# Optimization experiments

Measured on AMD Instinct MI355X. Metric: run time of the kernel, lower is better.

## Reference

```python
import jax, jax.numpy as jnp
import numpy as np

N_NODES = 100000
N_EDGES = 1000000
IN_DIM, HID_DIM, OUT_DIM = 64, 64, 128


def gcn_conv(x, W, b, src, dst, deg_inv_sqrt, n_nodes):
    # PyG GCNConv: x' = D^{-1/2} (A + I) D^{-1/2} (x W) + b
    xw = x @ W  # [N, out]
    norm = deg_inv_sqrt[src] * deg_inv_sqrt[dst]  # [E'] (edges incl. self-loops)
    msgs = xw[src] * norm[:, None]  # gather + scale, [E', out]
    out = jax.ops.segment_sum(msgs, dst, num_segments=n_nodes)
    return out + b


def setup_inputs() -> dict:
    key = jax.random.key(0)
    ks = jax.random.split(key, 8)
    x = jax.random.normal(ks[0], (N_NODES, IN_DIM), dtype=jnp.float32)
    edge_index = jax.random.randint(ks[1], (2, N_EDGES), 0, N_NODES, dtype=jnp.int64 if jax.config.read('jax_enable_x64') else jnp.int32)
    # Glorot-ish init for weights, zeros for biases (matches GCNConv defaults)
    def glorot(k, fan_in, fan_out):
        s = jnp.sqrt(6.0 / (fan_in + fan_out))
        return jax.random.uniform(k, (fan_in, fan_out), jnp.float32, -s, s)
    return {
        "x": x,
        "W1": glorot(ks[2], IN_DIM, HID_DIM), "b1": jnp.zeros((HID_DIM,), jnp.float32),
        "W2": glorot(ks[3], HID_DIM, HID_DIM), "b2": jnp.zeros((HID_DIM,), jnp.float32),
        "W3": glorot(ks[4], HID_DIM, OUT_DIM), "b3": jnp.zeros((OUT_DIM,), jnp.float32),
        "edge_index": edge_index,
    }


def reference(x, W1, b1, W2, b2, W3, b3, edge_index):
    n = x.shape[0]
    loop = jnp.arange(n, dtype=edge_index.dtype)
    src = jnp.concatenate([edge_index[0], loop])  # add self-loops
    dst = jnp.concatenate([edge_index[1], loop])
    deg = jax.ops.segment_sum(jnp.ones_like(dst, dtype=x.dtype), dst, num_segments=n)
    deg_inv_sqrt = jnp.where(deg > 0, jax.lax.rsqrt(deg), 0.0)
    # Dropout(p=0.5) is identity in eval mode
    h = jax.nn.relu(gcn_conv(x, W1, b1, src, dst, deg_inv_sqrt, n))
    h = jax.nn.relu(gcn_conv(h, W2, b2, src, dst, deg_inv_sqrt, n))
    return gcn_conv(h, W3, b3, src, dst, deg_inv_sqrt, n)
```

## Files before the change

### kernel.cpp

```cpp
#include <hip/hip_runtime.h>
#include <hip/hip_fp16.h>


#define NBMAX 512
#define EPB   4096


__global__ __launch_bounds__(256) void bin_hist(const int* __restrict__ dst,
                                                int* __restrict__ hist, int E, int NB) {
  __shared__ int cnt[NBMAX];
  for (int i = threadIdx.x; i < NB; i += 256) cnt[i] = 0;
  __syncthreads();
  int base = blockIdx.x * EPB;
  for (int it = 0; it < EPB; it += 256) {
    int e = base + it + threadIdx.x;
    if (e < E) atomicAdd(&cnt[dst[e] >> 8], 1);
  }
  __syncthreads();
  for (int i = threadIdx.x; i < NB; i += 256) hist[(size_t)blockIdx.x * NB + i] = cnt[i];
}

__global__ __launch_bounds__(256) void bucket_prefix(int* __restrict__ hist,
                                                     int* __restrict__ bucket_tot,
                                                     int nblk, int NB) {
  __shared__ int tmp[256];
  int b = blockIdx.x;
  int t = threadIdx.x;
  int v = (t < nblk) ? hist[(size_t)t * NB + b] : 0;
  tmp[t] = v;
  __syncthreads();
  for (int off = 1; off < 256; off <<= 1) {
    int a = (t >= off) ? tmp[t - off] : 0;
    __syncthreads();
    tmp[t] += a;
    __syncthreads();
  }
  if (t < nblk) hist[(size_t)t * NB + b] = tmp[t] - v;
  if (t == 255) bucket_tot[b] = tmp[255];
}

__global__ __launch_bounds__(512) void bucket_scan(const int* __restrict__ bucket_tot,
                                                   int* __restrict__ bucket_off, int NB, int E) {
  __shared__ int tmp[NBMAX];
  int t = threadIdx.x;
  int v = (t < NB) ? bucket_tot[t] : 0;
  tmp[t] = v;
  __syncthreads();
  for (int off = 1; off < 512; off <<= 1) {
    int a = (t >= off) ? tmp[t - off] : 0;
    __syncthreads();
    tmp[t] += a;
    __syncthreads();
  }
  if (t < NB) bucket_off[t] = tmp[t] - v;
  if (t == 0) bucket_off[NB] = E;
}

__global__ __launch_bounds__(256) void bin_scatter(const int* __restrict__ src,
                                                   const int* __restrict__ dst,
                                                   const int* __restrict__ chunk_excl,
                                                   const int* __restrict__ bucket_off,
                                                   int* __restrict__ pairs, int E, int NB) {
  __shared__ int cur[NBMAX];
  for (int i = threadIdx.x; i < NB; i += 256)
    cur[i] = bucket_off[i] + chunk_excl[(size_t)blockIdx.x * NB + i];
  __syncthreads();
  int base = blockIdx.x * EPB;
  for (int it = 0; it < EPB; it += 256) {
    int e = base + it + threadIdx.x;
    if (e < E) {
      int d = dst[e];
      int pos = atomicAdd(&cur[d >> 8], 1);
      pairs[pos] = src[e] | ((d & 255) << 17);
    }
  }
}

__device__ __forceinline__ unsigned int packh(float a, float b) {
  unsigned int lo = (unsigned int)__half_as_ushort(__float2half_rn(a));
  unsigned int hi = (unsigned int)__half_as_ushort(__float2half_rn(b));
  return lo | (hi << 16);
}

__device__ __forceinline__ void unpack_add(float& x0, float& x1, unsigned int u) {
  x0 += __half2float(__ushort_as_half((unsigned short)(u & 0xffffu)));
  x1 += __half2float(__ushort_as_half((unsigned short)(u >> 16)));
}

__global__ __launch_bounds__(256) void bucket_fill(const int* __restrict__ pairs,
                                                   const int* __restrict__ bucket_off,
                                                   int* __restrict__ row_ptr,
                                                   int* __restrict__ csr_src,
                                                   float* __restrict__ dis,
                                                   const float* __restrict__ x,
                                                   unsigned short* __restrict__ xs,
                                                   int n, int NB) {
  __shared__ int cnt[256];
  __shared__ int tmp[256];
  __shared__ int cur[256];
  __shared__ float sdis[256];
  int b = blockIdx.x;
  int t = threadIdx.x;
  int node_base = b << 8;
  int ebeg = bucket_off[b];
  int eend = bucket_off[b + 1];
  cnt[t] = 0;
  __syncthreads();
  for (int e = ebeg + t; e < eend; e += 256) {
    atomicAdd(&cnt[(pairs[e] >> 17) & 255], 1);
  }
  __syncthreads();
  int v = cnt[t];
  tmp[t] = v;
  __syncthreads();
  for (int off = 1; off < 256; off <<= 1) {
    int a = (t >= off) ? tmp[t - off] : 0;
    __syncthreads();
    tmp[t] += a;
    __syncthreads();
  }
  int excl = tmp[t] - v;
  int node = node_base + t;
  float s = rsqrtf((float)v + 1.0f);
  sdis[t] = s;
  if (node < n) {
    row_ptr[node] = ebeg + excl;
    dis[node] = s;
  }
  cur[t] = ebeg + excl;
  if (b == NB - 1 && t == 0) row_ptr[n] = eend;
  __syncthreads();
  for (int e = ebeg + t; e < eend; e += 256) {
    int p = pairs[e];
    int pos = atomicAdd(&cur[(p >> 17) & 255], 1);
    csr_src[pos] = p & 0x1FFFF;
  }
  int rows = n - node_base;
  if (rows > 256) rows = 256;
  for (int i = t; i < rows * 8; i += 256) {
    int r = i >> 3;
    float sc = sdis[r];
    const float4* p = (const float4*)(x + ((size_t)(node_base + r) * 64) + (i & 7) * 8);
    float4 f0 = p[0];
    float4 f1 = p[1];
    uint4 u;
    u.x = packh(f0.x * sc, f0.y * sc);
    u.y = packh(f0.z * sc, f0.w * sc);
    u.z = packh(f1.x * sc, f1.y * sc);
    u.w = packh(f1.z * sc, f1.w * sc);
    *(uint4*)(xs + (size_t)(node_base + r) * 64 + (i & 7) * 8) = u;
  }
}


template <bool RELU, bool SCALE, bool OUTH, int NCB>
__global__ __launch_bounds__(256, 4) void gcn_layer(
    const int* __restrict__ row_ptr, const int* __restrict__ csr_src,
    const unsigned short* __restrict__ in, const float* __restrict__ dis,
    const float* __restrict__ W, const float* __restrict__ Bv,
    float* __restrict__ yF, unsigned short* __restrict__ yH, int n) {
  __shared__ float Xs[64 * 68];
  __shared__ float Ws[64 * 64 * NCB];
  int tid = threadIdx.x;
  int rb = blockIdx.x * 64;

  for (int i = tid; i < 64 * 16 * NCB; i += 256) {
    int k = i / (16 * NCB);
    int cq = (i % (16 * NCB)) << 2;
    *(float4*)&Ws[k * (64 * NCB) + cq] = *(const float4*)&W[(size_t)k * (64 * NCB) + cq];
  }

  int l15 = tid & 15;
  int gbase = tid & 48;
  int grp = tid >> 4;
  for (int it = 0; it < 4; ++it) {
    int r = it * 16 + grp;
    int cl = min(rb + r, n - 1);
    int beg = row_ptr[cl];
    int end = row_ptr[cl + 1];

    float a0 = 0.f, a1 = 0.f, a2 = 0.f, a3 = 0.f;
    {
      uint2 q = *(const uint2*)(in + (size_t)cl * 64 + l15 * 4);
      unpack_add(a0, a1, q.x); unpack_add(a2, a3, q.y);
    }
    int k = beg;
    for (; k + 16 <= end; k += 16) {
      int idx = csr_src[k + l15];
#pragma unroll
      for (int rr = 0; rr < 16; rr += 2) {
        int s0 = __shfl(idx, gbase + rr);
        int s1 = __shfl(idx, gbase + rr + 1);
        uint2 q0 = *(const uint2*)(in + (size_t)s0 * 64 + l15 * 4);
        uint2 q1 = *(const uint2*)(in + (size_t)s1 * 64 + l15 * 4);
        unpack_add(a0, a1, q0.x); unpack_add(a2, a3, q0.y);
        unpack_add(a0, a1, q1.x); unpack_add(a2, a3, q1.y);
      }
    }
    int cnt = end - k;
    if (cnt > 0) {
      int ii = k + l15;
      int last = end - 1;
      ii = (ii < end) ? ii : last;
      int idx = csr_src[ii];
#pragma unroll
      for (int rr = 0; rr < 16; rr += 2) {
        int s0 = __shfl(idx, gbase + rr);
        int s1 = __shfl(idx, gbase + rr + 1);
        uint2 q0 = *(const uint2*)(in + (size_t)s0 * 64 + l15 * 4);
        uint2 q1 = *(const uint2*)(in + (size_t)s1 * 64 + l15 * 4);
        q0.x = (rr < cnt) ? q0.x : 0u;
        q0.y = (rr < cnt) ? q0.y : 0u;
        q1.x = (rr + 1 < cnt) ? q1.x : 0u;
        q1.y = (rr + 1 < cnt) ? q1.y : 0u;
        unpack_add(a0, a1, q0.x); unpack_add(a2, a3, q0.y);
        unpack_add(a0, a1, q1.x); unpack_add(a2, a3, q1.y);
      }
    }
    float sc = dis[cl];
    *(float4*)&Xs[r * 68 + l15 * 4] =
        make_float4(a0 * sc, a1 * sc, a2 * sc, a3 * sc);
  }
  __syncthreads();

  int r0 = (tid >> 4) << 2;
  int c0 = (tid & 15) << 2;
  int gr0 = rb + r0;

#pragma unroll
  for (int cb = 0; cb < NCB; ++cb) {
    float4 a0 = make_float4(0.f, 0.f, 0.f, 0.f);
    float4 a1 = a0, a2 = a0, a3 = a0;

#pragma unroll 2
    for (int kc = 0; kc < 64; kc += 4) {
      float4 x0 = *(const float4*)&Xs[(r0 + 0) * 68 + kc];
      float4 x1 = *(const float4*)&Xs[(r0 + 1) * 68 + kc];
      float4 x2 = *(const float4*)&Xs[(r0 + 2) * 68 + kc];
      float4 x3 = *(const float4*)&Xs[(r0 + 3) * 68 + kc];
      const float* wp = &Ws[(size_t)kc * (64 * NCB) + cb * 64 + c0];
      float4 w0 = *(const float4*)(wp + 0 * (64 * NCB));
      float4 w1 = *(const float4*)(wp + 1 * (64 * NCB));
      float4 w2 = *(const float4*)(wp + 2 * (64 * NCB));
      float4 w3 = *(const float4*)(wp + 3 * (64 * NCB));
      a0.x = fmaf(x0.x, w0.x, a0.x); a0.y = fmaf(x0.x, w0.y, a0.y);
      a0.z = fmaf(x0.x, w0.z, a0.z); a0.w = fmaf(x0.x, w0.w, a0.w);
      a0.x = fmaf(x0.y, w1.x, a0.x); a0.y = fmaf(x0.y, w1.y, a0.y);
      a0.z = fmaf(x0.y, w1.z, a0.z); a0.w = fmaf(x0.y, w1.w, a0.w);
      a0.x = fmaf(x0.z, w2.x, a0.x); a0.y = fmaf(x0.z, w2.y, a0.y);
      a0.z = fmaf(x0.z, w2.z, a0.z); a0.w = fmaf(x0.z, w2.w, a0.w);
      a0.x = fmaf(x0.w, w3.x, a0.x); a0.y = fmaf(x0.w, w3.y, a0.y);
      a0.z = fmaf(x0.w, w3.z, a0.z); a0.w = fmaf(x0.w, w3.w, a0.w);
      a1.x = fmaf(x1.x, w0.x, a1.x); a1.y = fmaf(x1.x, w0.y, a1.y);
      a1.z = fmaf(x1.x, w0.z, a1.z); a1.w = fmaf(x1.x, w0.w, a1.w);
      a1.x = fmaf(x1.y, w1.x, a1.x); a1.y = fmaf(x1.y, w1.y, a1.y);
      a1.z = fmaf(x1.y, w1.z, a1.z); a1.w = fmaf(x1.y, w1.w, a1.w);
      a1.x = fmaf(x1.z, w2.x, a1.x); a1.y = fmaf(x1.z, w2.y, a1.y);
      a1.z = fmaf(x1.z, w2.z, a1.z); a1.w = fmaf(x1.z, w2.w, a1.w);
      a1.x = fmaf(x1.w, w3.x, a1.x); a1.y = fmaf(x1.w, w3.y, a1.y);
      a1.z = fmaf(x1.w, w3.z, a1.z); a1.w = fmaf(x1.w, w3.w, a1.w);
      a2.x = fmaf(x2.x, w0.x, a2.x); a2.y = fmaf(x2.x, w0.y, a2.y);
      a2.z = fmaf(x2.x, w0.z, a2.z); a2.w = fmaf(x2.x, w0.w, a2.w);
      a2.x = fmaf(x2.y, w1.x, a2.x); a2.y = fmaf(x2.y, w1.y, a2.y);
      a2.z = fmaf(x2.y, w1.z, a2.z); a2.w = fmaf(x2.y, w1.w, a2.w);
      a2.x = fmaf(x2.z, w2.x, a2.x); a2.y = fmaf(x2.z, w2.y, a2.y);
      a2.z = fmaf(x2.z, w2.z, a2.z); a2.w = fmaf(x2.z, w2.w, a2.w);
      a2.x = fmaf(x2.w, w3.x, a2.x); a2.y = fmaf(x2.w, w3.y, a2.y);
      a2.z = fmaf(x2.w, w3.z, a2.z); a2.w = fmaf(x2.w, w3.w, a2.w);
      a3.x = fmaf(x3.x, w0.x, a3.x); a3.y = fmaf(x3.x, w0.y, a3.y);
      a3.z = fmaf(x3.x, w0.z, a3.z); a3.w = fmaf(x3.x, w0.w, a3.w);
      a3.x = fmaf(x3.y, w1.x, a3.x); a3.y = fmaf(x3.y, w1.y, a3.y);
      a3.z = fmaf(x3.y, w1.z, a3.z); a3.w = fmaf(x3.y, w1.w, a3.w);
      a3.x = fmaf(x3.z, w2.x, a3.x); a3.y = fmaf(x3.z, w2.y, a3.y);
      a3.z = fmaf(x3.z, w2.z, a3.z); a3.w = fmaf(x3.z, w2.w, a3.w);
      a3.x = fmaf(x3.w, w3.x, a3.x); a3.y = fmaf(x3.w, w3.y, a3.y);
      a3.z = fmaf(x3.w, w3.z, a3.z); a3.w = fmaf(x3.w, w3.w, a3.w);
    }

    float4 bb = *(const float4*)&Bv[cb * 64 + c0];
#pragma unroll
    for (int ri = 0; ri < 4; ++ri) {
      int gr = gr0 + ri;
      if (gr >= n) break;
      float4 v = (ri == 0) ? a0 : (ri == 1) ? a1 : (ri == 2) ? a2 : a3;
      v.x += bb.x; v.y += bb.y; v.z += bb.z; v.w += bb.w;
      if (RELU) {
        v.x = fmaxf(v.x, 0.f); v.y = fmaxf(v.y, 0.f);
        v.z = fmaxf(v.z, 0.f); v.w = fmaxf(v.w, 0.f);
      }
      if (SCALE) {
        float s = dis[gr];
        v.x *= s; v.y *= s; v.z *= s; v.w *= s;
      }
      if (OUTH) {
        uint2 u;
        u.x = packh(v.x, v.y);
        u.y = packh(v.z, v.w);
        *(uint2*)(yH + (size_t)gr * 64 + c0) = u;
      } else {
        *(float4*)&yF[(size_t)gr * (64 * NCB) + cb * 64 + c0] = v;
      }
    }
  }
}


extern "C" void kernel_launch(void* const* d_in, const int* in_sizes, int n_in,
                              void* d_out, int out_size, void* d_ws, size_t ws_size,
                              hipStream_t stream) {
  const float* x  = (const float*)d_in[0];
  const float* W1 = (const float*)d_in[1];
  const float* b1 = (const float*)d_in[2];
  const float* W2 = (const float*)d_in[3];
  const float* b2 = (const float*)d_in[4];
  const float* W3 = (const float*)d_in[5];
  const float* b3 = (const float*)d_in[6];
  const int*   ei = (const int*)d_in[7];

  const int n = in_sizes[0] / 64;
  const int E = in_sizes[7] / 2;
  const int* src = ei;
  const int* dst = ei + E;

  const int NB    = (n + 255) >> 8;
  const int nblkA = (E + EPB - 1) / EPB;

  float* dis = (float*)d_ws;
  unsigned short* bufA = (unsigned short*)(dis + n);
  unsigned short* bufB = bufA + (size_t)n * 64;
  int* row_ptr = (int*)(bufB + (size_t)n * 64);
  int* csr_src = row_ptr + (n + 2);
  int* pairs   = csr_src + E;
  int* hist       = pairs + E;
  int* bucket_tot = hist + (size_t)nblkA * NB;
  int* bucket_off = bucket_tot + NB;
  float* out = (float*)d_out;

  dim3 blk(256);
  int gL = (n + 63) / 64;

  bin_hist<<<nblkA, blk, 0, stream>>>(dst, hist, E, NB);
  bucket_prefix<<<NB, blk, 0, stream>>>(hist, bucket_tot, nblkA, NB);
  bucket_scan<<<1, 512, 0, stream>>>(bucket_tot, bucket_off, NB, E);
  bin_scatter<<<nblkA, blk, 0, stream>>>(src, dst, hist, bucket_off, pairs, E, NB);
  bucket_fill<<<NB, blk, 0, stream>>>(pairs, bucket_off, row_ptr, csr_src, dis, x, bufA, n, NB);

  gcn_layer<true, true, true, 1><<<gL, blk, 0, stream>>>(
      row_ptr, csr_src, bufA, dis, W1, b1, nullptr, bufB, n);

  gcn_layer<true, true, true, 1><<<gL, blk, 0, stream>>>(
      row_ptr, csr_src, bufB, dis, W2, b2, nullptr, bufA, n);

  gcn_layer<false, false, false, 2><<<gL, blk, 0, stream>>>(
      row_ptr, csr_src, bufA, dis, W3, b3, out, nullptr, n);
}
```

Measured before the change: 253.4 us.

## Halve rows per block, stage W per column block, unroll gather by four

Each layer block now handles 32 rows instead of 64, and only one 64x64 slice of W is kept in shared memory, reloaded per column block. This cuts LDS use and registers so the launch bound can target 6 blocks per SM instead of 4. The neighbor gather loop issues four row loads per iteration to raise memory-level parallelism. In exchange, twice as many blocks each reload W, and the NCB=2 layer adds extra syncs and global reloads of W.

```diff
diff --git a/kernel.cpp b/kernel.cpp
--- a/kernel.cpp
+++ b/kernel.cpp
@@ -154,26 +154,25 @@
 
 
 template <bool RELU, bool SCALE, bool OUTH, int NCB>
-__global__ __launch_bounds__(256, 4) void gcn_layer(
+__global__ __launch_bounds__(256, 6) void gcn_layer(
     const int* __restrict__ row_ptr, const int* __restrict__ csr_src,
     const unsigned short* __restrict__ in, const float* __restrict__ dis,
     const float* __restrict__ W, const float* __restrict__ Bv,
     float* __restrict__ yF, unsigned short* __restrict__ yH, int n) {
-  __shared__ float Xs[64 * 68];
-  __shared__ float Ws[64 * 64 * NCB];
+  __shared__ float Xs[32 * 68];
+  __shared__ float Ws[64 * 64];
   int tid = threadIdx.x;
-  int rb = blockIdx.x * 64;
-
-  for (int i = tid; i < 64 * 16 * NCB; i += 256) {
-    int k = i / (16 * NCB);
-    int cq = (i % (16 * NCB)) << 2;
-    *(float4*)&Ws[k * (64 * NCB) + cq] = *(const float4*)&W[(size_t)k * (64 * NCB) + cq];
+  int rb = blockIdx.x * 32;
+
+  for (int i = tid; i < 1024; i += 256) {
+    int k = i >> 4, cq = (i & 15) << 2;
+    *(float4*)&Ws[k * 64 + cq] = *(const float4*)&W[(size_t)k * (64 * NCB) + cq];
   }
 
   int l15 = tid & 15;
   int gbase = tid & 48;
   int grp = tid >> 4;
-  for (int it = 0; it < 4; ++it) {
+  for (int it = 0; it < 2; ++it) {
     int r = it * 16 + grp;
     int cl = min(rb + r, n - 1);
     int beg = row_ptr[cl];
@@ -188,13 +187,19 @@
     for (; k + 16 <= end; k += 16) {
       int idx = csr_src[k + l15];
 #pragma unroll
-      for (int rr = 0; rr < 16; rr += 2) {
+      for (int rr = 0; rr < 16; rr += 4) {
         int s0 = __shfl(idx, gbase + rr);
         int s1 = __shfl(idx, gbase + rr + 1);
+        int s2 = __shfl(idx, gbase + rr + 2);
+        int s3 = __shfl(idx, gbase + rr + 3);
         uint2 q0 = *(const uint2*)(in + (size_t)s0 * 64 + l15 * 4);
         uint2 q1 = *(const uint2*)(in + (size_t)s1 * 64 + l15 * 4);
+        uint2 q2 = *(const uint2*)(in + (size_t)s2 * 64 + l15 * 4);
+        uint2 q3 = *(const uint2*)(in + (size_t)s3 * 64 + l15 * 4);
         unpack_add(a0, a1, q0.x); unpack_add(a2, a3, q0.y);
         unpack_add(a0, a1, q1.x); unpack_add(a2, a3, q1.y);
+        unpack_add(a0, a1, q2.x); unpack_add(a2, a3, q2.y);
+        unpack_add(a0, a1, q3.x); unpack_add(a2, a3, q3.y);
       }
     }
     int cnt = end - k;
@@ -204,17 +209,27 @@
       ii = (ii < end) ? ii : last;
       int idx = csr_src[ii];
 #pragma unroll
-      for (int rr = 0; rr < 16; rr += 2) {
+      for (int rr = 0; rr < 16; rr += 4) {
         int s0 = __shfl(idx, gbase + rr);
         int s1 = __shfl(idx, gbase + rr + 1);
+        int s2 = __shfl(idx, gbase + rr + 2);
+        int s3 = __shfl(idx, gbase + rr + 3);
         uint2 q0 = *(const uint2*)(in + (size_t)s0 * 64 + l15 * 4);
         uint2 q1 = *(const uint2*)(in + (size_t)s1 * 64 + l15 * 4);
+        uint2 q2 = *(const uint2*)(in + (size_t)s2 * 64 + l15 * 4);
+        uint2 q3 = *(const uint2*)(in + (size_t)s3 * 64 + l15 * 4);
         q0.x = (rr < cnt) ? q0.x : 0u;
         q0.y = (rr < cnt) ? q0.y : 0u;
         q1.x = (rr + 1 < cnt) ? q1.x : 0u;
         q1.y = (rr + 1 < cnt) ? q1.y : 0u;
+        q2.x = (rr + 2 < cnt) ? q2.x : 0u;
+        q2.y = (rr + 2 < cnt) ? q2.y : 0u;
+        q3.x = (rr + 3 < cnt) ? q3.x : 0u;
+        q3.y = (rr + 3 < cnt) ? q3.y : 0u;
         unpack_add(a0, a1, q0.x); unpack_add(a2, a3, q0.y);
         unpack_add(a0, a1, q1.x); unpack_add(a2, a3, q1.y);
+        unpack_add(a0, a1, q2.x); unpack_add(a2, a3, q2.y);
+        unpack_add(a0, a1, q3.x); unpack_add(a2, a3, q3.y);
       }
     }
     float sc = dis[cl];
@@ -223,26 +238,33 @@
   }
   __syncthreads();
 
-  int r0 = (tid >> 4) << 2;
+  int r0 = (tid >> 4) << 1;
   int c0 = (tid & 15) << 2;
   int gr0 = rb + r0;
 
 #pragma unroll
   for (int cb = 0; cb < NCB; ++cb) {
+    if (cb > 0) {
+      __syncthreads();
+      for (int i = tid; i < 1024; i += 256) {
+        int k = i >> 4, cq = (i & 15) << 2;
+        *(float4*)&Ws[k * 64 + cq] =
+            *(const float4*)&W[(size_t)k * (64 * NCB) + cb * 64 + cq];
+      }
+      __syncthreads();
+    }
+
     float4 a0 = make_float4(0.f, 0.f, 0.f, 0.f);
-    float4 a1 = a0, a2 = a0, a3 = a0;
+    float4 a1 = a0;
 
 #pragma unroll 2
     for (int kc = 0; kc < 64; kc += 4) {
       float4 x0 = *(const float4*)&Xs[(r0 + 0) * 68 + kc];
       float4 x1 = *(const float4*)&Xs[(r0 + 1) * 68 + kc];
-      float4 x2 = *(const float4*)&Xs[(r0 + 2) * 68 + kc];
-      float4 x3 = *(const float4*)&Xs[(r0 + 3) * 68 + kc];
-      const float* wp = &Ws[(size_t)kc * (64 * NCB) + cb * 64 + c0];
-      float4 w0 = *(const float4*)(wp + 0 * (64 * NCB));
-      float4 w1 = *(const float4*)(wp + 1 * (64 * NCB));
-      float4 w2 = *(const float4*)(wp + 2 * (64 * NCB));
-      float4 w3 = *(const float4*)(wp + 3 * (64 * NCB));
+      float4 w0 = *(const float4*)&Ws[(kc + 0) * 64 + c0];
+      float4 w1 = *(const float4*)&Ws[(kc + 1) * 64 + c0];
+      float4 w2 = *(const float4*)&Ws[(kc + 2) * 64 + c0];
+      float4 w3 = *(const float4*)&Ws[(kc + 3) * 64 + c0];
       a0.x = fmaf(x0.x, w0.x, a0.x); a0.y = fmaf(x0.x, w0.y, a0.y);
       a0.z = fmaf(x0.x, w0.z, a0.z); a0.w = fmaf(x0.x, w0.w, a0.w);
       a0.x = fmaf(x0.y, w1.x, a0.x); a0.y = fmaf(x0.y, w1.y, a0.y);
@@ -259,30 +281,14 @@
       a1.z = fmaf(x1.z, w2.z, a1.z); a1.w = fmaf(x1.z, w2.w, a1.w);
       a1.x = fmaf(x1.w, w3.x, a1.x); a1.y = fmaf(x1.w, w3.y, a1.y);
       a1.z = fmaf(x1.w, w3.z, a1.z); a1.w = fmaf(x1.w, w3.w, a1.w);
-      a2.x = fmaf(x2.x, w0.x, a2.x); a2.y = fmaf(x2.x, w0.y, a2.y);
-      a2.z = fmaf(x2.x, w0.z, a2.z); a2.w = fmaf(x2.x, w0.w, a2.w);
-      a2.x = fmaf(x2.y, w1.x, a2.x); a2.y = fmaf(x2.y, w1.y, a2.y);
-      a2.z = fmaf(x2.y, w1.z, a2.z); a2.w = fmaf(x2.y, w1.w, a2.w);
-      a2.x = fmaf(x2.z, w2.x, a2.x); a2.y = fmaf(x2.z, w2.y, a2.y);
-      a2.z = fmaf(x2.z, w2.z, a2.z); a2.w = fmaf(x2.z, w2.w, a2.w);
-      a2.x = fmaf(x2.w, w3.x, a2.x); a2.y = fmaf(x2.w, w3.y, a2.y);
-      a2.z = fmaf(x2.w, w3.z, a2.z); a2.w = fmaf(x2.w, w3.w, a2.w);
-      a3.x = fmaf(x3.x, w0.x, a3.x); a3.y = fmaf(x3.x, w0.y, a3.y);
-      a3.z = fmaf(x3.x, w0.z, a3.z); a3.w = fmaf(x3.x, w0.w, a3.w);
-      a3.x = fmaf(x3.y, w1.x, a3.x); a3.y = fmaf(x3.y, w1.y, a3.y);
-      a3.z = fmaf(x3.y, w1.z, a3.z); a3.w = fmaf(x3.y, w1.w, a3.w);
-      a3.x = fmaf(x3.z, w2.x, a3.x); a3.y = fmaf(x3.z, w2.y, a3.y);
-      a3.z = fmaf(x3.z, w2.z, a3.z); a3.w = fmaf(x3.z, w2.w, a3.w);
-      a3.x = fmaf(x3.w, w3.x, a3.x); a3.y = fmaf(x3.w, w3.y, a3.y);
-      a3.z = fmaf(x3.w, w3.z, a3.z); a3.w = fmaf(x3.w, w3.w, a3.w);
     }
 
     float4 bb = *(const float4*)&Bv[cb * 64 + c0];
 #pragma unroll
-    for (int ri = 0; ri < 4; ++ri) {
+    for (int ri = 0; ri < 2; ++ri) {
       int gr = gr0 + ri;
       if (gr >= n) break;
-      float4 v = (ri == 0) ? a0 : (ri == 1) ? a1 : (ri == 2) ? a2 : a3;
+      float4 v = (ri == 0) ? a0 : a1;
       v.x += bb.x; v.y += bb.y; v.z += bb.z; v.w += bb.w;
       if (RELU) {
         v.x = fmaxf(v.x, 0.f); v.y = fmaxf(v.y, 0.f);
@@ -337,7 +343,7 @@
   float* out = (float*)d_out;
 
   dim3 blk(256);
-  int gL = (n + 63) / 64;
+  int gL = (n + 31) / 32;
 
   bin_hist<<<nblkA, blk, 0, stream>>>(dst, hist, E, NB);
   bucket_prefix<<<NB, blk, 0, stream>>>(hist, bucket_tot, nblkA, NB);
```

Result: no change. 256.5 us (+1.2%).
